# Performance work log

Hardware: AMD Instinct MI355X
Metric: run time of the kernel (lower is better)

Reference implementation:

```python
import jax, jax.numpy as jnp
from jax import lax
import numpy as np

DN = ('NCH', 'OIH', 'NCH')  # torch Conv1d layout


def _ddsc(x, pw, dws, gate):
    """DynamicDepthSeparableConv1d: pointwise conv -> gated sum of depthwise convs."""
    out = lax.conv_general_dilated(x, pw, (1,), 'VALID', dimension_numbers=DN)
    g = jax.nn.softmax(gate)
    y = None
    for i, w in enumerate(dws):
        k = w.shape[-1]
        p = (k - 1) // 2  # torch padding=(k-1)//2, 'same' length for odd k
        c = lax.conv_general_dilated(out, w, (1,), [(p, p)],
                                     feature_group_count=out.shape[1],
                                     dimension_numbers=DN)
        y = g[i] * c if y is None else y + g[i] * c
    return y


def setup_inputs() -> dict:
    key = jax.random.key(0)
    ks = jax.random.split(key, 16)
    B, QKC, VC, H, L = 16, 32, 1, 8, 1024

    def pn(k, shape, s):
        return jax.random.normal(k, shape, jnp.float32) * s

    return {
        'queries': pn(ks[0], (B, QKC, L), 1.0),
        'keys': pn(ks[1], (B, QKC, L), 1.0),
        'values': pn(ks[2], (B, VC, L), 1.0),
        # to_queries params
        'q_pw': pn(ks[3], (QKC * H, QKC, 1), 1.0 / np.sqrt(QKC)),
        'q_dw3': pn(ks[4], (QKC * H, 1, 3), 1.0 / np.sqrt(3.0)),
        'q_dw15': pn(ks[5], (QKC * H, 1, 15), 1.0 / np.sqrt(15.0)),
        'q_gate': jnp.array([0.5, 0.5], jnp.float32),
        # to_keys params (share_encoder=False -> separate weights)
        'k_pw': pn(ks[6], (QKC * H, QKC, 1), 1.0 / np.sqrt(QKC)),
        'k_dw3': pn(ks[7], (QKC * H, 1, 3), 1.0 / np.sqrt(3.0)),
        'k_dw15': pn(ks[8], (QKC * H, 1, 15), 1.0 / np.sqrt(15.0)),
        'k_gate': jnp.array([0.5, 0.5], jnp.float32),
        # to_values params
        'v_pw': pn(ks[9], (VC * H, VC, 1), 1.0),
        'v_dw3': pn(ks[10], (VC * H, 1, 3), 1.0 / np.sqrt(3.0)),
        'v_dw15': pn(ks[11], (VC * H, 1, 15), 1.0 / np.sqrt(15.0)),
        'v_gate': jnp.array([0.5, 0.5], jnp.float32),
        # unify_heads: Conv1d(h*v_c, v_c, 1) with bias
        'u_w': pn(ks[12], (VC, H * VC, 1), 1.0 / np.sqrt(H * VC)),
        'u_b': jnp.zeros((VC,), jnp.float32),
    }


def reference(queries, keys, values, q_pw, q_dw3, q_dw15, q_gate,
              k_pw, k_dw3, k_dw15, k_gate, v_pw, v_dw3, v_dw15, v_gate,
              u_w, u_b):
    B, qk_c, L = queries.shape
    _, v_c, _ = values.shape
    h = q_pw.shape[0] // qk_c

    # conv encoders -> split heads (channel layout matches torch .view(B,h,c,L))
    q = _ddsc(queries, q_pw, (q_dw3, q_dw15), q_gate).reshape(B * h, qk_c, L)
    k = _ddsc(keys, k_pw, (k_dw3, k_dw15), k_gate).reshape(B * h, qk_c, L)
    v = _ddsc(values, v_pw, (v_dw3, v_dw15), v_gate).reshape(B * h, v_c, L)

    q = q * (qk_c ** -0.25)
    k = k * (v_c ** -0.25)

    # kv_b > 1 branch: dot = K^T Q, softmax over QUERY positions (dim=2)
    dot = jax.nn.softmax(jnp.einsum('bcl,bcm->blm', k, q), axis=2)  # [B*h, Lk, Lq]
    out = jnp.einsum('bvl,blm->bvm', v, dot)  # [B*h, v_c, Lq]
    out = out.mean(axis=1)                    # [B*h, Lq]  (valid since v_c == 1)
    out = out.reshape(B, h * v_c, L)

    # unify_heads: 1x1 conv with bias
    out = jnp.einsum('bhl,oh->bol', out, u_w[:, :, 0]) + u_b[None, :, None]
    return out
```

## Files before the change

kernel.cpp:

```cpp
#include <hip/hip_runtime.h>
#include <math.h>


typedef __attribute__((ext_vector_type(8))) short bf16x8;
typedef __attribute__((ext_vector_type(16))) float f32x16;

__device__ inline ushort f32_to_bf16_rne(float f) {
    unsigned u = __builtin_bit_cast(unsigned, f);
    unsigned r = (u + 0x7FFFu + ((u >> 16) & 1u)) >> 16;
    return (ushort)r;
}
__device__ inline float bf16_hi_f32(ushort h) {
    unsigned u = ((unsigned)h) << 16;
    return __builtin_bit_cast(float, u);
}

__global__ __launch_bounds__(256) void enc_qk(
    const float* __restrict__ x,
    const float* __restrict__ pw,
    const float* __restrict__ dw3,
    const float* __restrict__ dw15,
    const float* __restrict__ gate,
    ushort* __restrict__ out,
    float scale)
{
    __shared__ float xs[32][280];
    __shared__ float wl[32][33];

    const int tid = threadIdx.x;
    const int lc = blockIdx.x, ot = blockIdx.y, b = blockIdx.z;
    const int l0 = lc << 8, ocb = ot << 5;

    for (int idx = tid; idx < 32 * 276; idx += 256) {
        const int ic = idx / 276, j = idx - ic * 276;
        const int gl = l0 - 8 + j;
        xs[ic][j] = (gl >= 0 && gl < 1024) ? x[(b * 32 + ic) * 1024 + gl] : 0.0f;
    }
    for (int idx = tid; idx < 1024; idx += 256)
        wl[idx >> 5][idx & 31] = pw[(ocb + (idx >> 5)) * 32 + (idx & 31)];
    __syncthreads();

    const int oc = tid & 31;
    const int t  = tid >> 5;

    float acc[48];
#pragma unroll
    for (int j = 0; j < 48; ++j) acc[j] = 0.0f;

#pragma unroll 1
    for (int ic = 0; ic < 32; ++ic) {
        const float4* xr = (const float4*)&xs[ic][t * 32];
        float4 xv[13];
#pragma unroll
        for (int j = 0; j < 13; ++j) xv[j] = xr[j];
        const float wv = wl[oc][ic];
#pragma unroll
        for (int j = 0; j < 48; ++j)
            acc[j] += wv * ((const float*)xv)[j + 1];
    }

    const float ge0 = gate[0], ge1 = gate[1];
    const float gm = fmaxf(ge0, ge1);
    const float e0 = __expf(ge0 - gm), e1 = __expf(ge1 - gm);
    const float g0 = e0 / (e0 + e1), g1 = e1 / (e0 + e1);

    float w3[3], w15[15];
#pragma unroll
    for (int d = 0; d < 3; ++d)  w3[d]  = dw3[(ocb + oc) * 3 + d];
#pragma unroll
    for (int d = 0; d < 15; ++d) w15[d] = dw15[(ocb + oc) * 15 + d];

    const long long rowbase = (long long)(b * 8 + ot) * 1024 + l0 + t * 32;
#pragma unroll
    for (int i = 0; i < 32; ++i) {
        float a3 = acc[i + 6] * w3[0] + acc[i + 7] * w3[1] + acc[i + 8] * w3[2];
        float a15 = 0.0f;
#pragma unroll
        for (int d = 0; d < 15; ++d) a15 += acc[i + d] * w15[d];
        const float y = (g0 * a3 + g1 * a15) * scale;
        const ushort hi = f32_to_bf16_rne(y);
        const ushort lo = f32_to_bf16_rne(y - bf16_hi_f32(hi));
        out[(rowbase + i) * 64 + oc] = hi;
        out[(rowbase + i) * 64 + 32 + oc] = lo;
    }
}

__global__ __launch_bounds__(256) void enc_v(
    const float* __restrict__ x, const float* __restrict__ pw,
    const float* __restrict__ dw3, const float* __restrict__ dw15,
    const float* __restrict__ gate, float* __restrict__ out)
{
    __shared__ float xs[1040];
    const int tid = threadIdx.x, b = blockIdx.x;

    for (int idx = tid; idx < 1040; idx += 256) {
        const int gl = idx - 8;
        xs[idx] = (gl >= 0 && gl < 1024) ? x[b * 1024 + gl] : 0.0f;
    }
    __syncthreads();

    const float ge0 = gate[0], ge1 = gate[1];
    const float gm = fmaxf(ge0, ge1);
    const float e0 = __expf(ge0 - gm), e1 = __expf(ge1 - gm);
    const float g0 = e0 / (e0 + e1), g1 = e1 / (e0 + e1);

    const int oc = tid >> 5, li0 = tid & 31;
    const float wp = pw[oc];
    float w3[3], w15[15];
#pragma unroll
    for (int d = 0; d < 3; ++d)  w3[d]  = dw3[oc * 3 + d];
#pragma unroll
    for (int d = 0; d < 15; ++d) w15[d] = dw15[oc * 15 + d];

    for (int i = 0; i < 32; ++i) {
        const int l = li0 + 32 * i, pc = l + 8;
        float a3 = 0.0f, a15 = 0.0f;
#pragma unroll
        for (int d = 0; d < 3; ++d)  a3  += xs[pc + d - 1] * w3[d];
#pragma unroll
        for (int d = 0; d < 15; ++d) a15 += xs[pc + d - 7] * w15[d];
        out[(b * 8 + oc) * 1024 + l] = wp * (g0 * a3 + g1 * a15);
    }
}

#define MFMA6(ACC0, ACC1)                                                      \
    ACC0 = __builtin_amdgcn_mfma_f32_32x32x16_bf16(a_h0, b_h0, ACC0, 0, 0, 0); \
    ACC1 = __builtin_amdgcn_mfma_f32_32x32x16_bf16(a_h1, b_h1, ACC1, 0, 0, 0); \
    ACC0 = __builtin_amdgcn_mfma_f32_32x32x16_bf16(a_l0, b_h0, ACC0, 0, 0, 0); \
    ACC1 = __builtin_amdgcn_mfma_f32_32x32x16_bf16(a_l1, b_h1, ACC1, 0, 0, 0); \
    ACC0 = __builtin_amdgcn_mfma_f32_32x32x16_bf16(a_h0, b_l0, ACC0, 0, 0, 0); \
    ACC1 = __builtin_amdgcn_mfma_f32_32x32x16_bf16(a_h1, b_l1, ACC1, 0, 0, 0);

__global__ __launch_bounds__(512, 2) void attn(
    const ushort* __restrict__ qt,
    const ushort* __restrict__ ktb,
    const float* __restrict__ ve,
    float* __restrict__ ho)
{
    __shared__ ushort qs[1024 * 64];
    __shared__ ushort ks[128 * 64];
    __shared__ float zpart[8][32];
    __shared__ float coef_l[128];

    const int tid = threadIdx.x;
    const int lane = tid & 63, wid = tid >> 6;
    const int bh = blockIdx.x & 127;
    const int lc = blockIdx.x >> 7;
    const int l0 = lc << 7;
    const int s = wid >> 1, h = wid & 1;
    const int l31 = lane & 31, hi5 = lane >> 5;

    {
        const uint4* src = (const uint4*)(qt + (size_t)bh * 65536);
        for (int idx = tid; idx < 8192; idx += 512) {
            const int row = idx >> 3, slot = idx & 7;
            const uint4 v = src[idx];
            *(uint4*)((char*)qs + row * 128 + ((slot ^ (row & 7)) << 4)) = v;
        }
        const uint4* ksrc = (const uint4*)(ktb + (size_t)bh * 65536 + (size_t)l0 * 64);
        for (int idx = tid; idx < 1024; idx += 512) {
            const int row = idx >> 3, slot = idx & 7;
            const uint4 v = ksrc[idx];
            *(uint4*)((char*)ks + row * 128 + ((slot ^ (row & 7)) << 4)) = v;
        }
    }
    __syncthreads();

    bf16x8 a_h0, a_h1, a_l0, a_l1;
    {
        const int arow = (s << 5) + l31;
        const int asw = (arow & 7) << 4;
        const char* kb = (const char*)ks + arow * 128;
        a_h0 = *(const bf16x8*)(kb + (((hi5 << 4) | 0)  ^ asw));
        a_h1 = *(const bf16x8*)(kb + (((hi5 << 4) | 32) ^ asw));
        a_l0 = *(const bf16x8*)(kb + (((hi5 << 4) | 64) ^ asw));
        a_l1 = *(const bf16x8*)(kb + (((hi5 << 4) | 96) ^ asw));
    }

    const char* qbase = (const char*)qs + ((h << 9) + l31) * 128;
    const int bsw = (l31 & 7) << 4;
    const int ob_h0 = ((hi5 << 4) | 0)  ^ bsw;
    const int ob_h1 = ((hi5 << 4) | 32) ^ bsw;
    const int ob_l0 = ((hi5 << 4) | 64) ^ bsw;
    const int ob_l1 = ((hi5 << 4) | 96) ^ bsw;

    float zacc[16];
#pragma unroll
    for (int r = 0; r < 16; ++r) zacc[r] = 0.0f;

#pragma unroll
    for (int t = 0; t < 16; ++t) {
        const bf16x8 b_h0 = *(const bf16x8*)(qbase + t * 4096 + ob_h0);
        const bf16x8 b_h1 = *(const bf16x8*)(qbase + t * 4096 + ob_h1);
        const bf16x8 b_l0 = *(const bf16x8*)(qbase + t * 4096 + ob_l0);
        const bf16x8 b_l1 = *(const bf16x8*)(qbase + t * 4096 + ob_l1);
        f32x16 acc0 = (f32x16)(0.0f);
        f32x16 acc1 = (f32x16)(0.0f);
        MFMA6(acc0, acc1)
#pragma unroll
        for (int r = 0; r < 16; ++r)
            zacc[r] += __expf(acc0[r] + acc1[r]);
    }

#pragma unroll
    for (int r = 0; r < 16; ++r) {
        float z = zacc[r];
        z += __shfl_xor(z, 1);  z += __shfl_xor(z, 2);  z += __shfl_xor(z, 4);
        z += __shfl_xor(z, 8);  z += __shfl_xor(z, 16);
        zacc[r] = z;
    }
    if (l31 == 0) {
#pragma unroll
        for (int r = 0; r < 16; ++r)
            zpart[wid][(r & 3) + ((r >> 2) << 3) + (hi5 << 2)] = zacc[r];
    }
    __syncthreads();

    if (tid < 128) {
        const int ss = tid >> 5, rr = tid & 31;
        const float Z = zpart[ss * 2][rr] + zpart[ss * 2 + 1][rr];
        coef_l[tid] = ve[bh * 1024 + l0 + tid] / Z;
    }
    __syncthreads();

    float coefr[16];
#pragma unroll
    for (int r = 0; r < 16; ++r)
        coefr[r] = coef_l[(s << 5) + (r & 3) + ((r >> 2) << 3) + (hi5 << 2)];

    float oacc[16];
#pragma unroll
    for (int t = 0; t < 16; ++t) {
        const bf16x8 b_h0 = *(const bf16x8*)(qbase + t * 4096 + ob_h0);
        const bf16x8 b_h1 = *(const bf16x8*)(qbase + t * 4096 + ob_h1);
        const bf16x8 b_l0 = *(const bf16x8*)(qbase + t * 4096 + ob_l0);
        const bf16x8 b_l1 = *(const bf16x8*)(qbase + t * 4096 + ob_l1);
        f32x16 acc0 = (f32x16)(0.0f);
        f32x16 acc1 = (f32x16)(0.0f);
        MFMA6(acc0, acc1)
        float p0 = 0.f, p1 = 0.f, p2 = 0.f, p3 = 0.f;
#pragma unroll
        for (int r = 0; r < 16; r += 4) {
            p0 += coefr[r + 0] * __expf(acc0[r + 0] + acc1[r + 0]);
            p1 += coefr[r + 1] * __expf(acc0[r + 1] + acc1[r + 1]);
            p2 += coefr[r + 2] * __expf(acc0[r + 2] + acc1[r + 2]);
            p3 += coefr[r + 3] * __expf(acc0[r + 3] + acc1[r + 3]);
        }
        oacc[t] = (p0 + p1) + (p2 + p3);
    }

#pragma unroll
    for (int t = 0; t < 16; ++t) oacc[t] += __shfl_xor(oacc[t], 32);

    float* outred = (float*)ks;
    if (lane < 32) {
#pragma unroll
        for (int t = 0; t < 16; ++t)
            outred[(wid << 9) + (t << 5) + l31] = oacc[t];
    }
    __syncthreads();

#pragma unroll
    for (int mmi = 0; mmi < 2; ++mmi) {
        const int mm = tid + (mmi << 9);
        const int hh = mm >> 9, ml = mm & 511;
        const float v = outred[(0 + hh) * 512 + ml] + outred[(2 + hh) * 512 + ml]
                      + outred[(4 + hh) * 512 + ml] + outred[(6 + hh) * 512 + ml];
        atomicAdd(&ho[bh * 1024 + mm], v);
    }
}

__global__ __launch_bounds__(256) void unify(
    const float* __restrict__ ho, const float* __restrict__ uw,
    const float* __restrict__ ub, float* __restrict__ out)
{
    const int idx = blockIdx.x * 256 + threadIdx.x;
    const int b = idx >> 10, l = idx & 1023;
    float acc = ub[0];
#pragma unroll
    for (int hh = 0; hh < 8; ++hh)
        acc += ho[(((b << 3) + hh) << 10) | l] * uw[hh];
    out[idx] = acc;
}

extern "C" void kernel_launch(void* const* d_in, const int* in_sizes, int n_in,
                              void* d_out, int out_size, void* d_ws, size_t ws_size,
                              hipStream_t stream)
{
    const float* queries = (const float*)d_in[0];
    const float* keys    = (const float*)d_in[1];
    const float* values  = (const float*)d_in[2];
    const float* q_pw    = (const float*)d_in[3];
    const float* q_dw3   = (const float*)d_in[4];
    const float* q_dw15  = (const float*)d_in[5];
    const float* q_gate  = (const float*)d_in[6];
    const float* k_pw    = (const float*)d_in[7];
    const float* k_dw3   = (const float*)d_in[8];
    const float* k_dw15  = (const float*)d_in[9];
    const float* k_gate  = (const float*)d_in[10];
    const float* v_pw    = (const float*)d_in[11];
    const float* v_dw3   = (const float*)d_in[12];
    const float* v_dw15  = (const float*)d_in[13];
    const float* v_gate  = (const float*)d_in[14];
    const float* u_w     = (const float*)d_in[15];
    const float* u_b     = (const float*)d_in[16];

    ushort* qt  = (ushort*)d_ws;
    ushort* ktb = qt + 8388608ull;
    float*  vef = (float*)(ktb + 8388608ull);
    float*  ho  = vef + 131072;

    dim3 egrid(4, 8, 16);
    enc_qk<<<egrid, 256, 0, stream>>>(queries, q_pw, q_dw3, q_dw15, q_gate,
                                      qt, 0.42044820762685725f);
    enc_qk<<<egrid, 256, 0, stream>>>(keys, k_pw, k_dw3, k_dw15, k_gate,
                                      ktb, 1.0f);
    enc_v<<<16, 256, 0, stream>>>(values, v_pw, v_dw3, v_dw15, v_gate, vef);

    hipMemsetAsync(ho, 0, 128 * 1024 * sizeof(float), stream);

    attn<<<1024, 512, 0, stream>>>(qt, ktb, vef, ho);

    unify<<<64, 256, 0, stream>>>(ho, u_w, u_b, (float*)d_out);
}
```

Baseline: 235.7 us.

## Single-pass attention storing exp values as bf16, with 16x16 MFMA and exp2

Rewrites the attention kernel so the K^T·Q scores are computed once per key chunk instead of twice. The exponentials are cached in registers as packed bf16, then reused to form the value-weighted sum after the normaliser is known. It folds log2(e) into the query scale so it can use the native exp2, switches to 16x16x32 MFMA tiles, and launches 256 blocks that each loop over four key chunks while loading Q once. This removes the duplicated MFMA and exp work and most of the repeated Q staging, but adds a 128-register array with spill risk and rounds probabilities to bf16.

```diff
diff --git a/kernel.cpp b/kernel.cpp
--- a/kernel.cpp
+++ b/kernel.cpp
@@ -3,7 +3,13 @@
 
 
 typedef __attribute__((ext_vector_type(8))) short bf16x8;
-typedef __attribute__((ext_vector_type(16))) float f32x16;
+typedef __attribute__((ext_vector_type(4))) float f32x4;
+
+#if __has_builtin(__builtin_amdgcn_exp2f)
+#define EXP2(x) __builtin_amdgcn_exp2f(x)
+#else
+#define EXP2(x) exp2f(x)
+#endif
 
 __device__ inline ushort f32_to_bf16_rne(float f) {
     unsigned u = __builtin_bit_cast(unsigned, f);
@@ -13,6 +19,11 @@
 __device__ inline float bf16_hi_f32(ushort h) {
     unsigned u = ((unsigned)h) << 16;
     return __builtin_bit_cast(float, u);
+}
+__device__ inline unsigned cvt_pk_bf16(float a, float b) {
+    unsigned r;
+    asm("v_cvt_pk_bf16_f32 %0, %1, %2" : "=v"(r) : "v"(a), "v"(b));
+    return r;
 }
 
 __global__ __launch_bounds__(256) void enc_qk(
@@ -123,14 +134,6 @@
     }
 }
 
-#define MFMA6(ACC0, ACC1)                                                      \
-    ACC0 = __builtin_amdgcn_mfma_f32_32x32x16_bf16(a_h0, b_h0, ACC0, 0, 0, 0); \
-    ACC1 = __builtin_amdgcn_mfma_f32_32x32x16_bf16(a_h1, b_h1, ACC1, 0, 0, 0); \
-    ACC0 = __builtin_amdgcn_mfma_f32_32x32x16_bf16(a_l0, b_h0, ACC0, 0, 0, 0); \
-    ACC1 = __builtin_amdgcn_mfma_f32_32x32x16_bf16(a_l1, b_h1, ACC1, 0, 0, 0); \
-    ACC0 = __builtin_amdgcn_mfma_f32_32x32x16_bf16(a_h0, b_l0, ACC0, 0, 0, 0); \
-    ACC1 = __builtin_amdgcn_mfma_f32_32x32x16_bf16(a_h1, b_l1, ACC1, 0, 0, 0);
-
 __global__ __launch_bounds__(512, 2) void attn(
     const ushort* __restrict__ qt,
     const ushort* __restrict__ ktb,
@@ -139,135 +142,100 @@
 {
     __shared__ ushort qs[1024 * 64];
     __shared__ ushort ks[128 * 64];
-    __shared__ float zpart[8][32];
-    __shared__ float coef_l[128];
+    __shared__ float vs[128];
 
     const int tid = threadIdx.x;
     const int lane = tid & 63, wid = tid >> 6;
-    const int bh = blockIdx.x & 127;
-    const int lc = blockIdx.x >> 7;
-    const int l0 = lc << 7;
-    const int s = wid >> 1, h = wid & 1;
-    const int l31 = lane & 31, hi5 = lane >> 5;
+    const int bh = blockIdx.x >> 1;
+    const int cs = (blockIdx.x & 1) << 2;
+    const int l15 = lane & 15, g = lane >> 4;
 
     {
         const uint4* src = (const uint4*)(qt + (size_t)bh * 65536);
-        for (int idx = tid; idx < 8192; idx += 512) {
-            const int row = idx >> 3, slot = idx & 7;
-            const uint4 v = src[idx];
+        for (int i = tid; i < 8192; i += 512) {
+            const int row = i >> 3, slot = i & 7;
+            const uint4 v = src[i];
             *(uint4*)((char*)qs + row * 128 + ((slot ^ (row & 7)) << 4)) = v;
         }
-        const uint4* ksrc = (const uint4*)(ktb + (size_t)bh * 65536 + (size_t)l0 * 64);
-        for (int idx = tid; idx < 1024; idx += 512) {
-            const int row = idx >> 3, slot = idx & 7;
-            const uint4 v = ksrc[idx];
-            *(uint4*)((char*)ks + row * 128 + ((slot ^ (row & 7)) << 4)) = v;
-        }
-    }
-    __syncthreads();
-
-    bf16x8 a_h0, a_h1, a_l0, a_l1;
-    {
-        const int arow = (s << 5) + l31;
-        const int asw = (arow & 7) << 4;
-        const char* kb = (const char*)ks + arow * 128;
-        a_h0 = *(const bf16x8*)(kb + (((hi5 << 4) | 0)  ^ asw));
-        a_h1 = *(const bf16x8*)(kb + (((hi5 << 4) | 32) ^ asw));
-        a_l0 = *(const bf16x8*)(kb + (((hi5 << 4) | 64) ^ asw));
-        a_l1 = *(const bf16x8*)(kb + (((hi5 << 4) | 96) ^ asw));
-    }
-
-    const char* qbase = (const char*)qs + ((h << 9) + l31) * 128;
-    const int bsw = (l31 & 7) << 4;
-    const int ob_h0 = ((hi5 << 4) | 0)  ^ bsw;
-    const int ob_h1 = ((hi5 << 4) | 32) ^ bsw;
-    const int ob_l0 = ((hi5 << 4) | 64) ^ bsw;
-    const int ob_l1 = ((hi5 << 4) | 96) ^ bsw;
-
-    float zacc[16];
-#pragma unroll
-    for (int r = 0; r < 16; ++r) zacc[r] = 0.0f;
-
-#pragma unroll
-    for (int t = 0; t < 16; ++t) {
-        const bf16x8 b_h0 = *(const bf16x8*)(qbase + t * 4096 + ob_h0);
-        const bf16x8 b_h1 = *(const bf16x8*)(qbase + t * 4096 + ob_h1);
-        const bf16x8 b_l0 = *(const bf16x8*)(qbase + t * 4096 + ob_l0);
-        const bf16x8 b_l1 = *(const bf16x8*)(qbase + t * 4096 + ob_l1);
-        f32x16 acc0 = (f32x16)(0.0f);
-        f32x16 acc1 = (f32x16)(0.0f);
-        MFMA6(acc0, acc1)
-#pragma unroll
-        for (int r = 0; r < 16; ++r)
-            zacc[r] += __expf(acc0[r] + acc1[r]);
-    }
-
-#pragma unroll
-    for (int r = 0; r < 16; ++r) {
-        float z = zacc[r];
-        z += __shfl_xor(z, 1);  z += __shfl_xor(z, 2);  z += __shfl_xor(z, 4);
-        z += __shfl_xor(z, 8);  z += __shfl_xor(z, 16);
-        zacc[r] = z;
-    }
-    if (l31 == 0) {
-#pragma unroll
-        for (int r = 0; r < 16; ++r)
-            zpart[wid][(r & 3) + ((r >> 2) << 3) + (hi5 << 2)] = zacc[r];
-    }
-    __syncthreads();
-
-    if (tid < 128) {
-        const int ss = tid >> 5, rr = tid & 31;
-        const float Z = zpart[ss * 2][rr] + zpart[ss * 2 + 1][rr];
-        coef_l[tid] = ve[bh * 1024 + l0 + tid] / Z;
-    }
-    __syncthreads();
-
-    float coefr[16];
-#pragma unroll
-    for (int r = 0; r < 16; ++r)
-        coefr[r] = coef_l[(s << 5) + (r & 3) + ((r >> 2) << 3) + (hi5 << 2)];
+    }
+
+    const int swz = (l15 & 7) << 4;
+    const char* qsb = (const char*)qs + l15 * 128;
+    const int ob_h = ((g << 4)     ) ^ swz;
+    const int ob_l = ((g << 4) | 64) ^ swz;
+    const char* ksb = (const char*)ks + (wid * 16 + l15) * 128;
 
     float oacc[16];
 #pragma unroll
-    for (int t = 0; t < 16; ++t) {
-        const bf16x8 b_h0 = *(const bf16x8*)(qbase + t * 4096 + ob_h0);
-        const bf16x8 b_h1 = *(const bf16x8*)(qbase + t * 4096 + ob_h1);
-        const bf16x8 b_l0 = *(const bf16x8*)(qbase + t * 4096 + ob_l0);
-        const bf16x8 b_l1 = *(const bf16x8*)(qbase + t * 4096 + ob_l1);
-        f32x16 acc0 = (f32x16)(0.0f);
-        f32x16 acc1 = (f32x16)(0.0f);
-        MFMA6(acc0, acc1)
-        float p0 = 0.f, p1 = 0.f, p2 = 0.f, p3 = 0.f;
-#pragma unroll
-        for (int r = 0; r < 16; r += 4) {
-            p0 += coefr[r + 0] * __expf(acc0[r + 0] + acc1[r + 0]);
-            p1 += coefr[r + 1] * __expf(acc0[r + 1] + acc1[r + 1]);
-            p2 += coefr[r + 2] * __expf(acc0[r + 2] + acc1[r + 2]);
-            p3 += coefr[r + 3] * __expf(acc0[r + 3] + acc1[r + 3]);
-        }
-        oacc[t] = (p0 + p1) + (p2 + p3);
-    }
-
-#pragma unroll
-    for (int t = 0; t < 16; ++t) oacc[t] += __shfl_xor(oacc[t], 32);
-
-    float* outred = (float*)ks;
-    if (lane < 32) {
-#pragma unroll
-        for (int t = 0; t < 16; ++t)
-            outred[(wid << 9) + (t << 5) + l31] = oacc[t];
-    }
-    __syncthreads();
-
-#pragma unroll
-    for (int mmi = 0; mmi < 2; ++mmi) {
-        const int mm = tid + (mmi << 9);
-        const int hh = mm >> 9, ml = mm & 511;
-        const float v = outred[(0 + hh) * 512 + ml] + outred[(2 + hh) * 512 + ml]
-                      + outred[(4 + hh) * 512 + ml] + outred[(6 + hh) * 512 + ml];
-        atomicAdd(&ho[bh * 1024 + mm], v);
-    }
+    for (int q = 0; q < 16; ++q) oacc[q] = 0.0f;
+
+    for (int c = 0; c < 4; ++c) {
+        const int l0 = (cs + c) << 7;
+        __syncthreads();
+        {
+            const uint4* ksrc = (const uint4*)(ktb + (size_t)bh * 65536 + (size_t)l0 * 64);
+            for (int i = tid; i < 1024; i += 512) {
+                const int row = i >> 3, slot = i & 7;
+                const uint4 v = ksrc[i];
+                *(uint4*)((char*)ks + row * 128 + ((slot ^ (row & 7)) << 4)) = v;
+            }
+            if (tid < 128) vs[tid] = ve[bh * 1024 + l0 + tid];
+        }
+        __syncthreads();
+
+        const bf16x8 a_hi = *(const bf16x8*)(ksb + (((g << 4)     ) ^ swz));
+        const bf16x8 a_lo = *(const bf16x8*)(ksb + (((g << 4) | 64) ^ swz));
+
+        unsigned p[128];
+        float z0 = 0.f, z1 = 0.f, z2 = 0.f, z3 = 0.f;
+#pragma unroll
+        for (int t = 0; t < 64; ++t) {
+            const bf16x8 b_hi = *(const bf16x8*)(qsb + t * 2048 + ob_h);
+            const bf16x8 b_lo = *(const bf16x8*)(qsb + t * 2048 + ob_l);
+            f32x4 acc = (f32x4)(0.0f);
+            acc = __builtin_amdgcn_mfma_f32_16x16x32_bf16(a_hi, b_hi, acc, 0, 0, 0);
+            acc = __builtin_amdgcn_mfma_f32_16x16x32_bf16(a_lo, b_hi, acc, 0, 0, 0);
+            acc = __builtin_amdgcn_mfma_f32_16x16x32_bf16(a_hi, b_lo, acc, 0, 0, 0);
+            const float e0 = EXP2(acc[0]);
+            const float e1 = EXP2(acc[1]);
+            const float e2 = EXP2(acc[2]);
+            const float e3 = EXP2(acc[3]);
+            z0 += e0; z1 += e1; z2 += e2; z3 += e3;
+            p[2 * t]     = cvt_pk_bf16(e0, e1);
+            p[2 * t + 1] = cvt_pk_bf16(e2, e3);
+        }
+
+#pragma unroll
+        for (int d = 1; d < 16; d <<= 1) {
+            z0 += __shfl_xor(z0, d);
+            z1 += __shfl_xor(z1, d);
+            z2 += __shfl_xor(z2, d);
+            z3 += __shfl_xor(z3, d);
+        }
+        const int rbase = wid * 16 + 4 * g;
+        const float c0 = vs[rbase + 0] / z0;
+        const float c1 = vs[rbase + 1] / z1;
+        const float c2 = vs[rbase + 2] / z2;
+        const float c3 = vs[rbase + 3] / z3;
+
+#pragma unroll
+        for (int t = 0; t < 64; ++t) {
+            const unsigned u0 = p[2 * t], u1 = p[2 * t + 1];
+            const float f0 = __builtin_bit_cast(float, u0 << 16);
+            const float f1 = __builtin_bit_cast(float, u0 & 0xFFFF0000u);
+            const float f2 = __builtin_bit_cast(float, u1 << 16);
+            const float f3 = __builtin_bit_cast(float, u1 & 0xFFFF0000u);
+            float part = c0 * f0 + c1 * f1 + c2 * f2 + c3 * f3;
+            part += __shfl_xor(part, 16);
+            part += __shfl_xor(part, 32);
+            oacc[t >> 2] += (g == (t & 3)) ? part : 0.0f;
+        }
+    }
+
+    float* hob = ho + bh * 1024;
+#pragma unroll
+    for (int q = 0; q < 16; ++q)
+        atomicAdd(&hob[((q << 2) + g) * 16 + l15], oacc[q]);
 }
 
 __global__ __launch_bounds__(256) void unify(
@@ -312,14 +280,14 @@
 
     dim3 egrid(4, 8, 16);
     enc_qk<<<egrid, 256, 0, stream>>>(queries, q_pw, q_dw3, q_dw15, q_gate,
-                                      qt, 0.42044820762685725f);
+                                      qt, 0.6065785440f);
     enc_qk<<<egrid, 256, 0, stream>>>(keys, k_pw, k_dw3, k_dw15, k_gate,
                                       ktb, 1.0f);
     enc_v<<<16, 256, 0, stream>>>(values, v_pw, v_dw3, v_dw15, v_gate, vef);
 
     hipMemsetAsync(ho, 0, 128 * 1024 * sizeof(float), stream);
 
-    attn<<<1024, 512, 0, stream>>>(qt, ktb, vef, ho);
+    attn<<<256, 512, 0, stream>>>(qt, ktb, vef, ho);
 
     unify<<<64, 256, 0, stream>>>(ho, u_w, u_b, (float*)d_out);
 }
```

New measurement: 209.7 us. 11.0% less time.
